# Kernel tuning notes

Measured on AMD Instinct MI355X. Metric: run time of the kernel, lower is better.

## Reference

```python
import jax, jax.numpy as jnp
import numpy as np

H = 16
D_MODEL = 2048
D_K = D_MODEL // H


def setup_inputs() -> dict:
    key = jax.random.key(0)
    ks = jax.random.split(key, 5)
    B, S = 4, 2048
    x = jax.random.normal(ks[0], (B, S, D_MODEL), dtype=jnp.float32)
    scale = 1.0 / np.sqrt(D_MODEL)
    Wq = jax.random.normal(ks[1], (D_MODEL, D_MODEL), dtype=jnp.float32) * scale
    Wk = jax.random.normal(ks[2], (D_MODEL, D_MODEL), dtype=jnp.float32) * scale
    Wv = jax.random.normal(ks[3], (D_MODEL, D_MODEL), dtype=jnp.float32) * scale
    Wo = jax.random.normal(ks[4], (D_MODEL, D_MODEL), dtype=jnp.float32) * scale
    return {"x": x, "Wq": Wq, "Wk": Wk, "Wv": Wv, "Wo": Wo, "use_mask": 1}


def reference(x, Wq, Wk, Wv, Wo, use_mask):
    B, S, _ = x.shape
    # nn.Linear with no bias: y = x @ W.T; then split heads -> [B, H, S, d_k]
    def proj(W):
        return (x @ W.T).reshape(B, S, H, D_K).transpose(0, 2, 1, 3)

    q, k, v = proj(Wq), proj(Wk), proj(Wv)
    scores = jnp.einsum("bhqd,bhkd->bhqk", q, k) / jnp.sqrt(jnp.float32(D_K))
    if use_mask:
        causal = jnp.tril(jnp.ones((S, S), dtype=bool))  # [S, S]
        scores = jnp.where(causal, scores, -jnp.inf)
    probs = jax.nn.softmax(scores, axis=-1)
    out = jnp.einsum("bhqk,bhkd->bhqd", probs, v)
    out = out.transpose(0, 2, 1, 3).reshape(B, S, H * D_K)
    return out @ Wo.T
```

## Files before the change

kernel.cpp:

```cpp
#include <hip/hip_runtime.h>
#include <hip/hip_bf16.h>

typedef __bf16 bf16_t;
typedef __bf16 bf16x8 __attribute__((ext_vector_type(8)));
typedef float f32x4 __attribute__((ext_vector_type(4)));

#define B_  4
#define S_  2048
#define H_  16
#define DK_ 128
#define DM_ 2048
#define BS_ (B_ * S_)

static __device__ __forceinline__ f32x4 mfma16(bf16x8 a, bf16x8 b, f32x4 c) {
  return __builtin_amdgcn_mfma_f32_16x16x32_bf16(a, b, c, 0, 0, 0);
}

static __device__ __forceinline__ void async_copy16(const bf16_t* g, bf16_t* l) {
  __builtin_amdgcn_global_load_lds(
      (const __attribute__((address_space(1))) void*)g,
      (__attribute__((address_space(3))) void*)l, 16, 0, 0);
}

template <int CTRL>
static __device__ __forceinline__ float dpp_rorf(float x) {
  return __builtin_bit_cast(float,
      __builtin_amdgcn_update_dpp(0, __builtin_bit_cast(int, x), CTRL, 0xF, 0xF, true));
}
static __device__ __forceinline__ float rowmax16(float r) {
  r = fmaxf(r, dpp_rorf<0x121>(r));
  r = fmaxf(r, dpp_rorf<0x122>(r));
  r = fmaxf(r, dpp_rorf<0x124>(r));
  r = fmaxf(r, dpp_rorf<0x128>(r));
  return r;
}
static __device__ __forceinline__ float rowsum16(float r) {
  r += dpp_rorf<0x121>(r);
  r += dpp_rorf<0x122>(r);
  r += dpp_rorf<0x124>(r);
  r += dpp_rorf<0x128>(r);
  return r;
}

struct ChainOn  { static constexpr bool v = true;  };
struct ChainOff { static constexpr bool v = false; };

__global__ __launch_bounds__(256) void cvt_bf16(const float* __restrict__ in,
                                                bf16_t* __restrict__ out, int n8) {
  int i = blockIdx.x * 256 + threadIdx.x;
  if (i < n8) {
    const float4* p = (const float4*)in + (size_t)i * 2;
    float4 f0 = p[0], f1 = p[1];
    bf16x8 r;
    r[0] = (bf16_t)f0.x; r[1] = (bf16_t)f0.y; r[2] = (bf16_t)f0.z; r[3] = (bf16_t)f0.w;
    r[4] = (bf16_t)f1.x; r[5] = (bf16_t)f1.y; r[6] = (bf16_t)f1.z; r[7] = (bf16_t)f1.w;
    ((bf16x8*)out)[i] = r;
  }
}

template <typename TC, bool VTOUT>
__global__ __launch_bounds__(256) void gemm_bt(const bf16_t* __restrict__ A,
                                               const bf16_t* __restrict__ B,
                                               TC* __restrict__ C,
                                               int M, int N, int K) {
  __shared__ bf16_t As[128 * 32];
  __shared__ bf16_t Bs[128 * 32];

  const int tid  = threadIdx.x;
  const int wave = tid >> 6;
  const int lane = tid & 63;
  const int quad = lane >> 4;
  const int l16  = lane & 15;
  const int wm   = (wave & 1) * 64;
  const int wn   = (wave >> 1) * 64;
  const int bm   = blockIdx.x * 128;
  const int bn   = blockIdx.y * 128;

  const int c0 = wave * 128 + lane;
  const int c1 = wave * 128 + 64 + lane;
  const int r0 = c0 >> 2, o0 = (c0 & 3) * 8;
  const int r1 = c1 >> 2, o1 = (c1 & 3) * 8;

  const bf16_t* Ar0 = A + (size_t)(bm + r0) * K + o0;
  const bf16_t* Ar1 = A + (size_t)(bm + r1) * K + o1;
  const bf16_t* Br0 = B + (size_t)(bn + r0) * K + o0;
  const bf16_t* Br1 = B + (size_t)(bn + r1) * K + o1;
  bf16_t* as0 = As + wave * 1024;
  bf16_t* as1 = As + wave * 1024 + 512;
  bf16_t* bs0 = Bs + wave * 1024;
  bf16_t* bs1 = Bs + wave * 1024 + 512;

  f32x4 acc[4][4];
#pragma unroll
  for (int i = 0; i < 4; ++i)
#pragma unroll
    for (int j = 0; j < 4; ++j) acc[i][j] = (f32x4){0.f, 0.f, 0.f, 0.f};

  for (int k0 = 0; k0 < K; k0 += 32) {
    __syncthreads();
    async_copy16(Ar0 + k0, as0);
    async_copy16(Ar1 + k0, as1);
    async_copy16(Br0 + k0, bs0);
    async_copy16(Br1 + k0, bs1);
    __syncthreads();

    bf16x8 af[4], bfr[4];
#pragma unroll
    for (int mt = 0; mt < 4; ++mt)
      af[mt] = *(const bf16x8*)(As + (wm + mt * 16 + l16) * 32 + quad * 8);
#pragma unroll
    for (int nt = 0; nt < 4; ++nt)
      bfr[nt] = *(const bf16x8*)(Bs + (wn + nt * 16 + l16) * 32 + quad * 8);
#pragma unroll
    for (int mt = 0; mt < 4; ++mt)
#pragma unroll
      for (int nt = 0; nt < 4; ++nt)
        acc[mt][nt] = mfma16(af[mt], bfr[nt], acc[mt][nt]);
  }

#pragma unroll
  for (int mt = 0; mt < 4; ++mt)
#pragma unroll
    for (int nt = 0; nt < 4; ++nt)
#pragma unroll
      for (int v = 0; v < 4; ++v) {
        int row = bm + wm + mt * 16 + quad * 4 + v;
        int col = bn + wn + nt * 16 + l16;
        if constexpr (VTOUT) {
          size_t o = (size_t)(((row >> 11) * 16 + (col >> 7)) * 128 + (col & 127)) * S_ +
                     (row & 2047);
          C[o] = (TC)acc[mt][nt][v];
        } else {
          C[(size_t)row * N + col] = (TC)acc[mt][nt][v];
        }
      }
}

__global__ __launch_bounds__(256, 2) void attn_kernel(const bf16_t* __restrict__ Q,
                                                      const bf16_t* __restrict__ K,
                                                      const bf16_t* __restrict__ VT,
                                                      bf16_t* __restrict__ O,
                                                      const int* __restrict__ use_mask) {
  __shared__ bf16_t Ks[2 * 64 * 128];
  __shared__ bf16_t Vs[2 * 128 * 64];
  __shared__ bf16_t Ps[2 * 4 * 16 * 64];

  const int tid  = threadIdx.x;
  const int wave = tid >> 6;
  const int lane = tid & 63;
  const int quad = lane >> 4;
  const int l16  = lane & 15;

  const int lid  = (int)(blockIdx.y * gridDim.x + blockIdx.x);
  const int xcd  = lid & 7;
  const int t8   = lid >> 3;
  const int bh   = xcd + ((t8 >> 4) << 3);
  const int pair = t8 & 15;
  const int qa   = 31 - pair;
  const int qc   = pair;
  const int b = bh >> 4, h = bh & 15;
  const int maskflag = *use_mask;

  const size_t qbaseA = ((size_t)b * S_ + (size_t)qa * 64) * DM_ + h * DK_;
  const size_t qbaseC = ((size_t)b * S_ + (size_t)qc * 64) * DM_ + h * DK_;

  int skO[4], svO[4];
#pragma unroll
  for (int p = 0; p < 4; ++p) {
    int rK = p * 16 + wave * 4 + quad;
    skO[p] = rK * DM_ + ((l16 ^ (rK & 7)) * 8);
    int dV = p * 32 + wave * 8 + (lane >> 3);
    svO[p] = dV * S_ + (((lane & 7) ^ (dV & 7)) * 8);
  }

  const bf16_t* Kbase = K + (size_t)b * S_ * DM_ + h * DK_;
  const bf16_t* Vbase = VT + (size_t)bh * DK_ * S_;

  auto stage_kv = [&](int j, int buf) __attribute__((always_inline)) {
    const bf16_t* kb = Kbase + (size_t)j * 64 * DM_;
    const bf16_t* vb = Vbase + (size_t)j * 64;
    bf16_t* kl = Ks + buf * 8192 + wave * 512;
    bf16_t* vl = Vs + buf * 8192 + wave * 512;
#pragma unroll
    for (int p = 0; p < 4; ++p) {
      async_copy16(kb + skO[p], kl + p * 2048);
      async_copy16(vb + svO[p], vl + p * 2048);
    }
  };

  bf16x8 qfA[4], qfC[4];
#pragma unroll
  for (int kk = 0; kk < 4; ++kk) {
    size_t ro = (size_t)(wave * 16 + l16) * DM_ + kk * 32 + quad * 8;
    qfA[kk] = *(const bf16x8*)(Q + qbaseA + ro);
    qfC[kk] = *(const bf16x8*)(Q + qbaseC + ro);
  }

  stage_kv(0, 0);

  f32x4 accA[8], accC[8];
#pragma unroll
  for (int i = 0; i < 8; ++i) {
    accA[i] = (f32x4){0.f, 0.f, 0.f, 0.f};
    accC[i] = (f32x4){0.f, 0.f, 0.f, 0.f};
  }
  float mA[4], lA[4], mC[4], lC[4];
#pragma unroll
  for (int v = 0; v < 4; ++v) {
    mA[v] = -INFINITY; lA[v] = 0.f;
    mC[v] = -INFINITY; lC[v] = 0.f;
  }

  bf16_t* PwA = Ps + wave * 1024;
  bf16_t* PwC = Ps + 4096 + wave * 1024;

  const float c1 = 0.08838834764831845f * 1.4426950408889634f;

  const int ntA = maskflag ? qa + 1 : (S_ / 64);
  const int ntC = maskflag ? qc + 1 : (S_ / 64);

  auto softmax_chain = [&](f32x4 (&s)[4], float (&mrow)[4], float (&lrow)[4],
                           f32x4 (&acc)[8], bf16_t* Pw, bool masked)
      __attribute__((always_inline)) {
#pragma unroll
    for (int v = 0; v < 4; ++v) {
      float x[4];
#pragma unroll
      for (int nt = 0; nt < 4; ++nt) {
        float y = s[nt][v] * c1;
        if (masked) {
          int kg = nt * 16 + l16;
          int qg = wave * 16 + quad * 4 + v;
          if (kg > qg) y = -INFINITY;
        }
        x[nt] = y;
      }
      float r = fmaxf(fmaxf(x[0], x[1]), fmaxf(x[2], x[3]));
      r = rowmax16(r);
      float m = mrow[v];
      if (r > m + 8.f) {
        float alpha = __builtin_amdgcn_exp2f(m - r);
        lrow[v] *= alpha;
#pragma unroll
        for (int dt = 0; dt < 8; ++dt) acc[dt][v] *= alpha;
        mrow[v] = r;
        m = r;
      }
      float rs = 0.f;
      int prow = quad * 4 + v;
#pragma unroll
      for (int nt = 0; nt < 4; ++nt) {
        float p = __builtin_amdgcn_exp2f(x[nt] - m);
        rs += p;
        Pw[prow * 64 + ((nt * 16 + l16) ^ ((prow & 7) << 3))] = (bf16_t)p;
      }
      lrow[v] += rowsum16(rs);
    }
  };

  auto body = [&](auto DOC, int cur, bool maskedA, bool maskedC)
      __attribute__((always_inline)) {
    constexpr bool doC = decltype(DOC)::v;
    const bf16_t* KsB = Ks + cur * 8192;
    const bf16_t* VsB = Vs + cur * 8192;

    f32x4 sA[4], sC[4];
#pragma unroll
    for (int nt = 0; nt < 4; ++nt) {
      sA[nt] = (f32x4){0.f, 0.f, 0.f, 0.f};
      sC[nt] = (f32x4){0.f, 0.f, 0.f, 0.f};
    }
    __builtin_amdgcn_s_setprio(1);
#pragma unroll
    for (int kk = 0; kk < 4; ++kk) {
#pragma unroll
      for (int nt = 0; nt < 4; ++nt) {
        bf16x8 kf = *(const bf16x8*)(KsB + (nt * 16 + l16) * 128 +
                                     ((kk * 32 + quad * 8) ^ ((l16 & 7) << 3)));
        sA[nt] = mfma16(qfA[kk], kf, sA[nt]);
        if constexpr (doC) sC[nt] = mfma16(qfC[kk], kf, sC[nt]);
      }
    }
    __builtin_amdgcn_s_setprio(0);

    softmax_chain(sA, mA, lA, accA, PwA, maskedA);
    if constexpr (doC) softmax_chain(sC, mC, lC, accC, PwC, maskedC);

    __builtin_amdgcn_s_setprio(1);
#pragma unroll
    for (int kk = 0; kk < 2; ++kk) {
      bf16x8 pfA = *(const bf16x8*)(PwA + l16 * 64 +
                                    ((kk * 32 + quad * 8) ^ ((l16 & 7) << 3)));
      bf16x8 pfC = {};
      if constexpr (doC)
        pfC = *(const bf16x8*)(PwC + l16 * 64 +
                               ((kk * 32 + quad * 8) ^ ((l16 & 7) << 3)));
#pragma unroll
      for (int dt = 0; dt < 8; ++dt) {
        bf16x8 vf = *(const bf16x8*)(VsB + (dt * 16 + l16) * 64 +
                                     ((kk * 32 + quad * 8) ^ ((l16 & 7) << 3)));
        accA[dt] = mfma16(pfA, vf, accA[dt]);
        if constexpr (doC) accC[dt] = mfma16(pfC, vf, accC[dt]);
      }
    }
    __builtin_amdgcn_s_setprio(0);
  };

  __syncthreads();

  for (int t = 0; t < ntA; ++t) {
    const int cur = t & 1;
    if (t + 1 < ntA) stage_kv(t + 1, cur ^ 1);
    const bool mAf = maskflag && (t == qa);
    if (t < ntC)
      body(ChainOn{},  cur, mAf, maskflag && (t == qc));
    else
      body(ChainOff{}, cur, mAf, false);
    __syncthreads();
  }

  auto epilogue = [&](f32x4 (&acc)[8], float (&lrow)[4], size_t qbase)
      __attribute__((always_inline)) {
    float rl[4];
#pragma unroll
    for (int v = 0; v < 4; ++v) rl[v] = __builtin_amdgcn_rcpf(lrow[v]);
#pragma unroll
    for (int dt = 0; dt < 8; ++dt)
#pragma unroll
      for (int v = 0; v < 4; ++v) {
        int qr = wave * 16 + quad * 4 + v;
        O[qbase + (size_t)qr * DM_ + dt * 16 + l16] = (bf16_t)(acc[dt][v] * rl[v]);
      }
  };
  epilogue(accA, lA, qbaseA);
  epilogue(accC, lC, qbaseC);
}

extern "C" void kernel_launch(void* const* d_in, const int* in_sizes, int n_in,
                              void* d_out, int out_size, void* d_ws, size_t ws_size,
                              hipStream_t stream) {
  const float* x  = (const float*)d_in[0];
  const float* Wq = (const float*)d_in[1];
  const float* Wk = (const float*)d_in[2];
  const float* Wv = (const float*)d_in[3];
  const float* Wo = (const float*)d_in[4];
  const int* use_mask = (const int*)d_in[5];
  float* out = (float*)d_out;

  const size_t TSZ = (size_t)BS_ * DM_;
  const size_t WSZ = (size_t)DM_ * DM_;
  bf16_t* Qb  = (bf16_t*)d_ws;
  bf16_t* Kb  = Qb + TSZ;
  bf16_t* Vt  = Kb + TSZ;
  bf16_t* xb  = Vt + TSZ;
  bf16_t* Ob  = xb;
  bf16_t* Wob = Vt;
  bf16_t* wq = (bf16_t*)d_out;
  bf16_t* wk = wq + WSZ;
  bf16_t* wv = wk + WSZ;

  cvt_bf16<<<(int)(TSZ / 8 / 256), 256, 0, stream>>>(x,  xb, (int)(TSZ / 8));
  cvt_bf16<<<(int)(WSZ / 8 / 256), 256, 0, stream>>>(Wq, wq, (int)(WSZ / 8));
  cvt_bf16<<<(int)(WSZ / 8 / 256), 256, 0, stream>>>(Wk, wk, (int)(WSZ / 8));
  cvt_bf16<<<(int)(WSZ / 8 / 256), 256, 0, stream>>>(Wv, wv, (int)(WSZ / 8));

  dim3 gGemm(BS_ / 128, DM_ / 128);
  gemm_bt<bf16_t, false><<<gGemm, 256, 0, stream>>>(xb, wq, Qb, BS_, DM_, DM_);
  gemm_bt<bf16_t, false><<<gGemm, 256, 0, stream>>>(xb, wk, Kb, BS_, DM_, DM_);
  gemm_bt<bf16_t, true ><<<gGemm, 256, 0, stream>>>(xb, wv, Vt, BS_, DM_, DM_);

  dim3 gA(16, 64);
  attn_kernel<<<gA, 256, 0, stream>>>(Qb, Kb, Vt, Ob, use_mask);

  cvt_bf16<<<(int)(WSZ / 8 / 256), 256, 0, stream>>>(Wo, Wob, (int)(WSZ / 8));
  gemm_bt<float, false><<<gGemm, 256, 0, stream>>>(Ob, Wob, out, BS_, DM_, DM_);
}
```

Measured before the change: 690.6 us.

## Replace 128x128 GEMM with pipelined 256x256 tile, swizzled LDS, XCD-aware mapping

```diff
diff --git a/kernel.cpp b/kernel.cpp
--- a/kernel.cpp
+++ b/kernel.cpp
@@ -59,67 +59,141 @@
 }
 
 template <typename TC, bool VTOUT>
-__global__ __launch_bounds__(256) void gemm_bt(const bf16_t* __restrict__ A,
-                                               const bf16_t* __restrict__ B,
-                                               TC* __restrict__ C,
-                                               int M, int N, int K) {
-  __shared__ bf16_t As[128 * 32];
-  __shared__ bf16_t Bs[128 * 32];
+__global__ __launch_bounds__(512, 2) void gemm256(const bf16_t* __restrict__ A,
+                                                  const bf16_t* __restrict__ B,
+                                                  TC* __restrict__ C,
+                                                  int M, int N, int K) {
+  __shared__ bf16_t Ab[2][2][256 * 32];
+  __shared__ bf16_t Bb[2][2][256 * 32];
 
   const int tid  = threadIdx.x;
   const int wave = tid >> 6;
   const int lane = tid & 63;
   const int quad = lane >> 4;
   const int l16  = lane & 15;
-  const int wm   = (wave & 1) * 64;
-  const int wn   = (wave >> 1) * 64;
-  const int bm   = blockIdx.x * 128;
-  const int bn   = blockIdx.y * 128;
-
-  const int c0 = wave * 128 + lane;
-  const int c1 = wave * 128 + 64 + lane;
-  const int r0 = c0 >> 2, o0 = (c0 & 3) * 8;
-  const int r1 = c1 >> 2, o1 = (c1 & 3) * 8;
-
-  const bf16_t* Ar0 = A + (size_t)(bm + r0) * K + o0;
-  const bf16_t* Ar1 = A + (size_t)(bm + r1) * K + o1;
-  const bf16_t* Br0 = B + (size_t)(bn + r0) * K + o0;
-  const bf16_t* Br1 = B + (size_t)(bn + r1) * K + o1;
-  bf16_t* as0 = As + wave * 1024;
-  bf16_t* as1 = As + wave * 1024 + 512;
-  bf16_t* bs0 = Bs + wave * 1024;
-  bf16_t* bs1 = Bs + wave * 1024 + 512;
-
-  f32x4 acc[4][4];
-#pragma unroll
-  for (int i = 0; i < 4; ++i)
+  const int wm   = (wave >> 2) * 128;
+  const int wn   = (wave & 3) * 64;
+
+  const int bid = (int)blockIdx.x;
+  const int xcd = bid & 7;
+  const int idx = bid >> 3;
+  const int bm  = (xcd * 4 + (idx >> 3)) * 256;
+  const int bn  = (idx & 7) * 256;
+
+  const int p_ = lane & 3;
+  const int r0 = wave * 32 + (lane >> 2);
+  const int r1 = r0 + 16;
+  const int s0 = (r0 + (r0 >> 2)) & 3;
+  const int s1 = (r1 + (r1 >> 2)) & 3;
+  const size_t aO0 = (size_t)(bm + r0) * K + (p_ ^ s0) * 8;
+  const size_t aO1 = (size_t)(bm + r1) * K + (p_ ^ s1) * 8;
+  const size_t bO0 = (size_t)(bn + r0) * K + (p_ ^ s0) * 8;
+  const size_t bO1 = (size_t)(bn + r1) * K + (p_ ^ s1) * 8;
+  const int ldsW = wave * 1024;
+
+  auto stA = [&](int slot, int kh, int kt) __attribute__((always_inline)) {
+    const int c = kt * 64 + kh * 32;
+    bf16_t* d = &Ab[slot][kh][ldsW];
+    async_copy16(A + aO0 + c, d);
+    async_copy16(A + aO1 + c, d + 512);
+  };
+  auto stB = [&](int slot, int kh, int kt) __attribute__((always_inline)) {
+    const int c = kt * 64 + kh * 32;
+    bf16_t* d = &Bb[slot][kh][ldsW];
+    async_copy16(B + bO0 + c, d);
+    async_copy16(B + bO1 + c, d + 512);
+  };
+
+  const int sw  = (l16 + (l16 >> 2)) & 3;
+  const int qs  = (quad ^ sw) * 8;
+  const int arB = (wm + l16) * 32 + qs;
+  const int brB = (wn + l16) * 32 + qs;
+
+  f32x4 acc[8][4];
+#pragma unroll
+  for (int i = 0; i < 8; ++i)
 #pragma unroll
     for (int j = 0; j < 4; ++j) acc[i][j] = (f32x4){0.f, 0.f, 0.f, 0.f};
 
-  for (int k0 = 0; k0 < K; k0 += 32) {
-    __syncthreads();
-    async_copy16(Ar0 + k0, as0);
-    async_copy16(Ar1 + k0, as1);
-    async_copy16(Br0 + k0, bs0);
-    async_copy16(Br1 + k0, bs1);
-    __syncthreads();
-
+  const int NT = K >> 6;
+
+  stA(0, 0, 0); stB(0, 0, 0);
+  stA(0, 1, 0); stB(0, 1, 0);
+  { int k1 = NT > 1 ? 1 : 0; stA(1, 0, k1); stB(1, 0, k1); }
+  asm volatile("s_waitcnt vmcnt(8)" ::: "memory");
+  __syncthreads();
+
+  for (int t = 0; t < NT; ++t) {
+    const int cur = t & 1, nxt = cur ^ 1;
+    const int tp1 = (t + 1 < NT) ? t + 1 : NT - 1;
+    const int tp2 = (t + 2 < NT) ? t + 2 : NT - 1;
     bf16x8 af[4], bfr[4];
-#pragma unroll
-    for (int mt = 0; mt < 4; ++mt)
-      af[mt] = *(const bf16x8*)(As + (wm + mt * 16 + l16) * 32 + quad * 8);
-#pragma unroll
-    for (int nt = 0; nt < 4; ++nt)
-      bfr[nt] = *(const bf16x8*)(Bs + (wn + nt * 16 + l16) * 32 + quad * 8);
-#pragma unroll
-    for (int mt = 0; mt < 4; ++mt)
-#pragma unroll
-      for (int nt = 0; nt < 4; ++nt)
-        acc[mt][nt] = mfma16(af[mt], bfr[nt], acc[mt][nt]);
-  }
-
-#pragma unroll
-  for (int mt = 0; mt < 4; ++mt)
+
+#pragma unroll
+    for (int i = 0; i < 4; ++i)
+      af[i] = *(const bf16x8*)(&Ab[cur][0][arB + i * 512]);
+#pragma unroll
+    for (int n = 0; n < 4; ++n)
+      bfr[n] = *(const bf16x8*)(&Bb[cur][0][brB + n * 512]);
+    stA(nxt, 1, tp1);
+    __syncthreads();
+    __builtin_amdgcn_s_setprio(1);
+#pragma unroll
+    for (int i = 0; i < 4; ++i)
+#pragma unroll
+      for (int n = 0; n < 4; ++n) acc[i][n] = mfma16(af[i], bfr[n], acc[i][n]);
+    __builtin_amdgcn_s_setprio(0);
+    __syncthreads();
+
+#pragma unroll
+    for (int i = 0; i < 4; ++i)
+      af[i] = *(const bf16x8*)(&Ab[cur][0][arB + 2048 + i * 512]);
+    stB(nxt, 1, tp1);
+    __syncthreads();
+    __builtin_amdgcn_s_setprio(1);
+#pragma unroll
+    for (int i = 0; i < 4; ++i)
+#pragma unroll
+      for (int n = 0; n < 4; ++n)
+        acc[4 + i][n] = mfma16(af[i], bfr[n], acc[4 + i][n]);
+    __builtin_amdgcn_s_setprio(0);
+    asm volatile("s_waitcnt vmcnt(8)" ::: "memory");
+    __syncthreads();
+
+#pragma unroll
+    for (int i = 0; i < 4; ++i)
+      af[i] = *(const bf16x8*)(&Ab[cur][1][arB + i * 512]);
+#pragma unroll
+    for (int n = 0; n < 4; ++n)
+      bfr[n] = *(const bf16x8*)(&Bb[cur][1][brB + n * 512]);
+    stA(cur, 0, tp2);
+    __syncthreads();
+    __builtin_amdgcn_s_setprio(1);
+#pragma unroll
+    for (int i = 0; i < 4; ++i)
+#pragma unroll
+      for (int n = 0; n < 4; ++n) acc[i][n] = mfma16(af[i], bfr[n], acc[i][n]);
+    __builtin_amdgcn_s_setprio(0);
+    __syncthreads();
+
+#pragma unroll
+    for (int i = 0; i < 4; ++i)
+      af[i] = *(const bf16x8*)(&Ab[cur][1][arB + 2048 + i * 512]);
+    stB(cur, 0, tp2);
+    __syncthreads();
+    __builtin_amdgcn_s_setprio(1);
+#pragma unroll
+    for (int i = 0; i < 4; ++i)
+#pragma unroll
+      for (int n = 0; n < 4; ++n)
+        acc[4 + i][n] = mfma16(af[i], bfr[n], acc[4 + i][n]);
+    __builtin_amdgcn_s_setprio(0);
+    asm volatile("s_waitcnt vmcnt(8)" ::: "memory");
+    __syncthreads();
+  }
+
+#pragma unroll
+  for (int mt = 0; mt < 8; ++mt)
 #pragma unroll
     for (int nt = 0; nt < 4; ++nt)
 #pragma unroll
@@ -364,14 +438,14 @@
   cvt_bf16<<<(int)(WSZ / 8 / 256), 256, 0, stream>>>(Wk, wk, (int)(WSZ / 8));
   cvt_bf16<<<(int)(WSZ / 8 / 256), 256, 0, stream>>>(Wv, wv, (int)(WSZ / 8));
 
-  dim3 gGemm(BS_ / 128, DM_ / 128);
-  gemm_bt<bf16_t, false><<<gGemm, 256, 0, stream>>>(xb, wq, Qb, BS_, DM_, DM_);
-  gemm_bt<bf16_t, false><<<gGemm, 256, 0, stream>>>(xb, wk, Kb, BS_, DM_, DM_);
-  gemm_bt<bf16_t, true ><<<gGemm, 256, 0, stream>>>(xb, wv, Vt, BS_, DM_, DM_);
+  dim3 gG(256);
+  gemm256<bf16_t, false><<<gG, 512, 0, stream>>>(xb, wq, Qb, BS_, DM_, DM_);
+  gemm256<bf16_t, false><<<gG, 512, 0, stream>>>(xb, wk, Kb, BS_, DM_, DM_);
+  gemm256<bf16_t, true ><<<gG, 512, 0, stream>>>(xb, wv, Vt, BS_, DM_, DM_);
 
   dim3 gA(16, 64);
   attn_kernel<<<gA, 256, 0, stream>>>(Qb, Kb, Vt, Ob, use_mask);
 
   cvt_bf16<<<(int)(WSZ / 8 / 256), 256, 0, stream>>>(Wo, Wob, (int)(WSZ / 8));
-  gemm_bt<float, false><<<gGemm, 256, 0, stream>>>(Ob, Wob, out, BS_, DM_, DM_);
-}
+  gemm256<float, false><<<gG, 512, 0, stream>>>(Ob, Wob, out, BS_, DM_, DM_);
+}
```

Result: no change. 690.9 us (+0.0%).

## Rewrite projection GEMMs with 256x256 tiles, 4-stage async pipeline, fused QKV launch

Applied to the files above, without the earlier changes.

```diff
diff --git a/kernel.cpp b/kernel.cpp
--- a/kernel.cpp
+++ b/kernel.cpp
@@ -21,6 +21,8 @@
       (const __attribute__((address_space(1))) void*)g,
       (__attribute__((address_space(3))) void*)l, 16, 0, 0);
 }
+
+#define BARRIER() asm volatile("s_barrier" ::: "memory")
 
 template <int CTRL>
 static __device__ __forceinline__ float dpp_rorf(float x) {
@@ -58,82 +60,123 @@
   }
 }
 
-template <typename TC, bool VTOUT>
-__global__ __launch_bounds__(256) void gemm_bt(const bf16_t* __restrict__ A,
-                                               const bf16_t* __restrict__ B,
-                                               TC* __restrict__ C,
-                                               int M, int N, int K) {
-  __shared__ bf16_t As[128 * 32];
-  __shared__ bf16_t Bs[128 * 32];
-
+template <typename TC>
+static __device__ __forceinline__ void gemm_body(
+    const bf16_t* __restrict__ A, const bf16_t* __restrict__ B, TC* __restrict__ C,
+    bool vtout, int b256, bf16_t (&Ab)[4][8192], bf16_t (&Bb)[4][8192]) {
   const int tid  = threadIdx.x;
   const int wave = tid >> 6;
   const int lane = tid & 63;
   const int quad = lane >> 4;
   const int l16  = lane & 15;
-  const int wm   = (wave & 1) * 64;
-  const int wn   = (wave >> 1) * 64;
-  const int bm   = blockIdx.x * 128;
-  const int bn   = blockIdx.y * 128;
-
-  const int c0 = wave * 128 + lane;
-  const int c1 = wave * 128 + 64 + lane;
-  const int r0 = c0 >> 2, o0 = (c0 & 3) * 8;
-  const int r1 = c1 >> 2, o1 = (c1 & 3) * 8;
-
-  const bf16_t* Ar0 = A + (size_t)(bm + r0) * K + o0;
-  const bf16_t* Ar1 = A + (size_t)(bm + r1) * K + o1;
-  const bf16_t* Br0 = B + (size_t)(bn + r0) * K + o0;
-  const bf16_t* Br1 = B + (size_t)(bn + r1) * K + o1;
-  bf16_t* as0 = As + wave * 1024;
-  bf16_t* as1 = As + wave * 1024 + 512;
-  bf16_t* bs0 = Bs + wave * 1024;
-  bf16_t* bs1 = Bs + wave * 1024 + 512;
-
-  f32x4 acc[4][4];
-#pragma unroll
-  for (int i = 0; i < 4; ++i)
+  const int wm   = (wave >> 2) * 128;
+  const int wn   = (wave & 3) * 64;
+
+  const int xcd = b256 & 7;
+  const int idx = b256 >> 3;
+  const int bm  = (xcd * 4 + (idx >> 3)) * 256;
+  const int bn  = (idx & 7) * 256;
+  const int K   = DM_;
+
+  const int r0 = wave * 16 + (lane >> 2);
+  const int r1 = r0 + 128;
+  const int s0 = (r0 + (r0 >> 2)) & 3;
+  const int s1 = (r1 + (r1 >> 2)) & 3;
+  const size_t aO0 = (size_t)(bm + r0) * K + ((lane & 3) ^ s0) * 8;
+  const size_t aO1 = (size_t)(bm + r1) * K + ((lane & 3) ^ s1) * 8;
+  const size_t bO0 = (size_t)(bn + r0) * K + ((lane & 3) ^ s0) * 8;
+  const size_t bO1 = (size_t)(bn + r1) * K + ((lane & 3) ^ s1) * 8;
+  const int dst0 = wave * 512;
+  const int dst1 = 4096 + wave * 512;
+
+  auto stage = [&](int slot, int kt) __attribute__((always_inline)) {
+    const size_t c = (size_t)kt * 32;
+    async_copy16(A + aO0 + c, &Ab[slot][dst0]);
+    async_copy16(A + aO1 + c, &Ab[slot][dst1]);
+    async_copy16(B + bO0 + c, &Bb[slot][dst0]);
+    async_copy16(B + bO1 + c, &Bb[slot][dst1]);
+  };
+
+  const int sw = (l16 + (l16 >> 2)) & 3;
+  const int qs = (quad ^ sw) * 8;
+
+  f32x4 acc[8][4];
+#pragma unroll
+  for (int i = 0; i < 8; ++i)
 #pragma unroll
     for (int j = 0; j < 4; ++j) acc[i][j] = (f32x4){0.f, 0.f, 0.f, 0.f};
 
-  for (int k0 = 0; k0 < K; k0 += 32) {
-    __syncthreads();
-    async_copy16(Ar0 + k0, as0);
-    async_copy16(Ar1 + k0, as1);
-    async_copy16(Br0 + k0, bs0);
-    async_copy16(Br1 + k0, bs1);
-    __syncthreads();
-
-    bf16x8 af[4], bfr[4];
-#pragma unroll
-    for (int mt = 0; mt < 4; ++mt)
-      af[mt] = *(const bf16x8*)(As + (wm + mt * 16 + l16) * 32 + quad * 8);
-#pragma unroll
-    for (int nt = 0; nt < 4; ++nt)
-      bfr[nt] = *(const bf16x8*)(Bs + (wn + nt * 16 + l16) * 32 + quad * 8);
-#pragma unroll
-    for (int mt = 0; mt < 4; ++mt)
-#pragma unroll
-      for (int nt = 0; nt < 4; ++nt)
-        acc[mt][nt] = mfma16(af[mt], bfr[nt], acc[mt][nt]);
-  }
-
-#pragma unroll
-  for (int mt = 0; mt < 4; ++mt)
+  const int NT = K >> 5;
+
+  stage(0, 0); stage(1, 1); stage(2, 2);
+  asm volatile("s_waitcnt vmcnt(8)" ::: "memory");
+  BARRIER();
+
+  for (int t = 0; t < NT; ++t) {
+    const bf16_t* Abuf = Ab[t & 3];
+    const bf16_t* Bbuf = Bb[t & 3];
+    const int kt = (t + 3 < NT) ? t + 3 : NT - 1;
+    stage((t + 3) & 3, kt);
+
+    bf16x8 af[8], bfr[4];
+#pragma unroll
+    for (int j = 0; j < 8; ++j)
+      af[j] = *(const bf16x8*)(&Abuf[(wm + j * 16 + l16) * 32 + qs]);
+#pragma unroll
+    for (int n = 0; n < 4; ++n)
+      bfr[n] = *(const bf16x8*)(&Bbuf[(wn + n * 16 + l16) * 32 + qs]);
+
+    __builtin_amdgcn_s_setprio(1);
+#pragma unroll
+    for (int j = 0; j < 8; ++j)
+#pragma unroll
+      for (int n = 0; n < 4; ++n)
+        acc[j][n] = mfma16(af[j], bfr[n], acc[j][n]);
+    __builtin_amdgcn_s_setprio(0);
+
+    asm volatile("s_waitcnt vmcnt(8)" ::: "memory");
+    BARRIER();
+  }
+
+  asm volatile("s_waitcnt vmcnt(0)" ::: "memory");
+
+#pragma unroll
+  for (int mt = 0; mt < 8; ++mt)
 #pragma unroll
     for (int nt = 0; nt < 4; ++nt)
 #pragma unroll
       for (int v = 0; v < 4; ++v) {
         int row = bm + wm + mt * 16 + quad * 4 + v;
         int col = bn + wn + nt * 16 + l16;
-        if constexpr (VTOUT) {
+        if (vtout) {
           size_t o = (size_t)(((row >> 11) * 16 + (col >> 7)) * 128 + (col & 127)) * S_ +
                      (row & 2047);
           C[o] = (TC)acc[mt][nt][v];
         } else {
-          C[(size_t)row * N + col] = (TC)acc[mt][nt][v];
+          C[(size_t)row * DM_ + col] = (TC)acc[mt][nt][v];
         }
       }
+}
+
+__global__ __launch_bounds__(512, 2) void qkv_gemm(
+    const bf16_t* __restrict__ xb, const bf16_t* __restrict__ wq,
+    const bf16_t* __restrict__ wk, const bf16_t* __restrict__ wv,
+    bf16_t* __restrict__ Qb, bf16_t* __restrict__ Kb, bf16_t* __restrict__ Vt) {
+  __shared__ bf16_t Ab[4][8192];
+  __shared__ bf16_t Bb[4][8192];
+  const int seg  = (int)blockIdx.x >> 8;
+  const int b256 = (int)blockIdx.x & 255;
+  const bf16_t* W = (seg == 0) ? wq : (seg == 1) ? wk : wv;
+  bf16_t* C       = (seg == 0) ? Qb : (seg == 1) ? Kb : Vt;
+  gemm_body<bf16_t>(xb, W, C, seg == 2, b256, Ab, Bb);
+}
+
+__global__ __launch_bounds__(512, 2) void out_gemm(
+    const bf16_t* __restrict__ Ob, const bf16_t* __restrict__ Wob,
+    float* __restrict__ out) {
+  __shared__ bf16_t Ab[4][8192];
+  __shared__ bf16_t Bb[4][8192];
+  gemm_body<float>(Ob, Wob, out, false, (int)blockIdx.x, Ab, Bb);
 }
 
 __global__ __launch_bounds__(256, 2) void attn_kernel(const bf16_t* __restrict__ Q,
@@ -364,14 +407,11 @@
   cvt_bf16<<<(int)(WSZ / 8 / 256), 256, 0, stream>>>(Wk, wk, (int)(WSZ / 8));
   cvt_bf16<<<(int)(WSZ / 8 / 256), 256, 0, stream>>>(Wv, wv, (int)(WSZ / 8));
 
-  dim3 gGemm(BS_ / 128, DM_ / 128);
-  gemm_bt<bf16_t, false><<<gGemm, 256, 0, stream>>>(xb, wq, Qb, BS_, DM_, DM_);
-  gemm_bt<bf16_t, false><<<gGemm, 256, 0, stream>>>(xb, wk, Kb, BS_, DM_, DM_);
-  gemm_bt<bf16_t, true ><<<gGemm, 256, 0, stream>>>(xb, wv, Vt, BS_, DM_, DM_);
+  qkv_gemm<<<dim3(768), 512, 0, stream>>>(xb, wq, wk, wv, Qb, Kb, Vt);
 
   dim3 gA(16, 64);
   attn_kernel<<<gA, 256, 0, stream>>>(Qb, Kb, Vt, Ob, use_mask);
 
   cvt_bf16<<<(int)(WSZ / 8 / 256), 256, 0, stream>>>(Wo, Wob, (int)(WSZ / 8));
-  gemm_bt<float, false><<<gGemm, 256, 0, stream>>>(Ob, Wob, out, BS_, DM_, DM_);
-}
+  out_gemm<<<dim3(256), 512, 0, stream>>>(Ob, Wob, out);
+}
```

Result: faster. 654.9 us (-5.2%).
